# Performance work log

Hardware: AMD Instinct MI355X
Metric: run time of the kernel (lower is better)

Reference implementation:

```python
import jax, jax.numpy as jnp
import numpy as np

TOKENS, D_IN, D_OUT, RANK = 16384, 4096, 4096, 512

def setup_inputs() -> dict:
    key = jax.random.key(0)
    k1, k2, k3, k4 = jax.random.split(key, 4)
    x = jax.random.normal(k1, (TOKENS, D_IN), dtype=jnp.float32)
    U = jax.random.normal(k2, (D_OUT, RANK), dtype=jnp.float32) * 0.02
    sigma = jax.random.uniform(k3, (RANK,), dtype=jnp.float32)
    V = jax.random.normal(k4, (D_IN, RANK), dtype=jnp.float32) * 0.02
    return {"x": x, "U": U, "sigma": sigma, "V": V}

def reference(x, U, sigma, V):
    # W = U @ diag(sigma) @ V.T  (shape [out, in]); out = x @ W.T
    # diag(sigma) contraction expressed as a column scale of U (same math).
    W = (U * sigma[None, :]) @ V.T          # [out, in]
    return x @ W.T                          # [tokens, out]
```

## Files before the change

### kernel.cpp

```cpp
#include <hip/hip_runtime.h>

typedef __bf16 bf16;
typedef __bf16 bf16x4 __attribute__((ext_vector_type(4)));
typedef __bf16 bf16x8 __attribute__((ext_vector_type(8)));
typedef float  f32x4  __attribute__((ext_vector_type(4)));

#define TOKENS 16384
#define D_IN   4096
#define D_OUT  4096
#define RANK   512

__device__ inline void gload_lds16(const bf16* g, bf16* l) {
    __builtin_amdgcn_global_load_lds((const __attribute__((address_space(1))) void*)g,
                                     (__attribute__((address_space(3))) void*)l,
                                     16, 0, 0);
}

__global__ __launch_bounds__(256) void vt_scale(const float* __restrict__ V,
                                                const float* __restrict__ sg,
                                                bf16* __restrict__ Vst) {
    __shared__ float tile[64][65];
    const int tx = threadIdx.x & 63;
    const int ty = threadIdx.x >> 6;
    const int kb = blockIdx.x * 64;
    const int rb = blockIdx.y * 64;
    const float s = sg[rb + tx];
#pragma unroll
    for (int i = ty; i < 64; i += 4)
        tile[i][tx] = V[(size_t)(kb + i) * RANK + rb + tx] * s;
    __syncthreads();
#pragma unroll
    for (int i = ty; i < 64; i += 4) {
        int r = rb + i;
        int kp = kb + (tx ^ ((r & 7) << 3));
        Vst[(size_t)r * D_IN + kp] = (bf16)tile[tx][i];
    }
}

__global__ __launch_bounds__(256) void cvt_bf16_4(const float* __restrict__ in,
                                                  bf16* __restrict__ o, int n4) {
    int i = blockIdx.x * 256 + threadIdx.x;
    if (i < n4) {
        f32x4 v = *(const f32x4*)(in + (size_t)i * 4);
        bf16x4 b = { (bf16)v[0], (bf16)v[1], (bf16)v[2], (bf16)v[3] };
        *(bf16x4*)(o + (size_t)i * 4) = b;
    }
}

__global__ __launch_bounds__(256, 2) void gemm1_pipe(const float* __restrict__ A,
                                                     const bf16* __restrict__ B,
                                                     bf16* __restrict__ T,
                                                     int M, int N, int K) {
    __shared__ bf16 Al[2][128 * 64];
    __shared__ bf16 Bl[2][128 * 64];

    const int t  = threadIdx.x;
    const int l  = t & 63;
    const int w  = t >> 6;
    const int wr = w >> 1, wc = w & 1;
    const int lr = l & 15;
    const int kg = l >> 4;
    const int sxor = (l & 7) << 3;

    const int nwg = gridDim.x;
    const int bid = blockIdx.x;
    const int cpx = nwg >> 3;
    const int swz = (bid & 7) * cpx + (bid >> 3);
    const int ntn = N >> 7;
    const int tm  = (swz / ntn) << 7;
    const int tn  = (swz % ntn) << 7;

    const int arow  = t >> 4;
    const int acg   = t & 15;
    const int awxor = (arow & 7) << 3;
    const float* Ap = A + (size_t)(tm + arow) * K + acg * 4;
    const bf16* Bp  = B + (size_t)(tn + (t >> 3)) * K + (t & 7) * 8;

    f32x4 acc[4][4] = {};
    f32x4 ra[8];

#pragma unroll
    for (int c = 0; c < 8; ++c)
        ra[c] = *(const f32x4*)(Ap + (size_t)(c * 16) * K);
#pragma unroll
    for (int c = 0; c < 4; ++c)
        gload_lds16(Bp + (size_t)(c * 32) * K, &Bl[0][(c * 256 + t) * 8]);
#pragma unroll
    for (int c = 0; c < 8; ++c) {
        bf16x4 b = { (bf16)ra[c][0], (bf16)ra[c][1], (bf16)ra[c][2], (bf16)ra[c][3] };
        *(bf16x4*)&Al[0][(c * 16 + arow) * 64 + ((acg * 4) ^ awxor)] = b;
    }
    asm volatile("s_waitcnt vmcnt(0) lgkmcnt(0)" ::: "memory");
    __builtin_amdgcn_s_barrier();

    int cb = 0;
    for (int kt = 0; kt < K - 64; kt += 64) {
        const int nb = cb ^ 1;
#pragma unroll
        for (int c = 0; c < 8; ++c)
            ra[c] = *(const f32x4*)(Ap + kt + 64 + (size_t)(c * 16) * K);
#pragma unroll
        for (int c = 0; c < 4; ++c)
            gload_lds16(Bp + kt + 64 + (size_t)(c * 32) * K, &Bl[nb][(c * 256 + t) * 8]);

#pragma unroll
        for (int ks = 0; ks < 2; ++ks) {
            bf16x8 af[4], bfr[4];
#pragma unroll
            for (int f = 0; f < 4; ++f) {
                af[f]  = *(const bf16x8*)&Al[cb][(wr * 64 + f * 16 + lr) * 64 + ((ks * 32 + kg * 8) ^ sxor)];
                bfr[f] = *(const bf16x8*)&Bl[cb][(wc * 64 + f * 16 + lr) * 64 + ((ks * 32 + kg * 8) ^ sxor)];
            }
#pragma unroll
            for (int fm = 0; fm < 4; ++fm)
#pragma unroll
                for (int fn = 0; fn < 4; ++fn)
                    acc[fm][fn] = __builtin_amdgcn_mfma_f32_16x16x32_bf16(
                        af[fm], bfr[fn], acc[fm][fn], 0, 0, 0);
        }

#pragma unroll
        for (int c = 0; c < 8; ++c) {
            bf16x4 b = { (bf16)ra[c][0], (bf16)ra[c][1], (bf16)ra[c][2], (bf16)ra[c][3] };
            *(bf16x4*)&Al[nb][(c * 16 + arow) * 64 + ((acg * 4) ^ awxor)] = b;
        }
        asm volatile("s_waitcnt vmcnt(0) lgkmcnt(0)" ::: "memory");
        __builtin_amdgcn_s_barrier();
        cb = nb;
    }

#pragma unroll
    for (int ks = 0; ks < 2; ++ks) {
        bf16x8 af[4], bfr[4];
#pragma unroll
        for (int f = 0; f < 4; ++f) {
            af[f]  = *(const bf16x8*)&Al[cb][(wr * 64 + f * 16 + lr) * 64 + ((ks * 32 + kg * 8) ^ sxor)];
            bfr[f] = *(const bf16x8*)&Bl[cb][(wc * 64 + f * 16 + lr) * 64 + ((ks * 32 + kg * 8) ^ sxor)];
        }
#pragma unroll
        for (int fm = 0; fm < 4; ++fm)
#pragma unroll
            for (int fn = 0; fn < 4; ++fn)
                acc[fm][fn] = __builtin_amdgcn_mfma_f32_16x16x32_bf16(
                    af[fm], bfr[fn], acc[fm][fn], 0, 0, 0);
    }

    const int r0 = tm + wr * 64 + kg * 4;
    const int c0 = tn + wc * 64 + lr;
#pragma unroll
    for (int fm = 0; fm < 4; ++fm)
#pragma unroll
        for (int fn = 0; fn < 4; ++fn)
#pragma unroll
            for (int r = 0; r < 4; ++r)
                T[(size_t)(r0 + fm * 16 + r) * N + (c0 + fn * 16)] = (bf16)acc[fm][fn][r];
}

__global__ __launch_bounds__(256) void gemm2_bt(const bf16* __restrict__ A,
                                                const bf16* __restrict__ B,
                                                float* __restrict__ out,
                                                int M, int N, int K) {
    __shared__ bf16 Al[128 * 64];
    __shared__ bf16 Bl[128 * 64];

    const int t  = threadIdx.x;
    const int l  = t & 63;
    const int w  = t >> 6;
    const int wr = w >> 1, wc = w & 1;
    const int lr = l & 15;
    const int kg = l >> 4;

    const int nwg = gridDim.x;
    const int bid = blockIdx.x;
    const int cpx = nwg >> 3;
    const int swz = (bid & 7) * cpx + (bid >> 3);
    const int ntn = N >> 7;
    const int tm  = (swz / ntn) << 7;
    const int tn  = (swz % ntn) << 7;

    f32x4 acc[4][4] = {};

    for (int kt = 0; kt < K; kt += 64) {
#pragma unroll
        for (int c = 0; c < 4; ++c) {
            int i = c * 256 + t;
            gload_lds16(A + (size_t)(tm + (i >> 3)) * K + kt + (i & 7) * 8, &Al[i * 8]);
        }
#pragma unroll
        for (int c = 0; c < 4; ++c) {
            int i = c * 256 + t;
            gload_lds16(B + (size_t)(tn + (i >> 3)) * K + kt + (i & 7) * 8, &Bl[i * 8]);
        }
        __syncthreads();

#pragma unroll
        for (int ks = 0; ks < 2; ++ks) {
            bf16x8 af[4], bfr[4];
#pragma unroll
            for (int f = 0; f < 4; ++f) {
                af[f]  = *(const bf16x8*)&Al[(wr * 64 + f * 16 + lr) * 64 + ks * 32 + kg * 8];
                bfr[f] = *(const bf16x8*)&Bl[(wc * 64 + f * 16 + lr) * 64 + ks * 32 + kg * 8];
            }
#pragma unroll
            for (int fm = 0; fm < 4; ++fm)
#pragma unroll
                for (int fn = 0; fn < 4; ++fn)
                    acc[fm][fn] = __builtin_amdgcn_mfma_f32_16x16x32_bf16(
                        af[fm], bfr[fn], acc[fm][fn], 0, 0, 0);
        }
        __syncthreads();
    }

    const int r0 = tm + wr * 64 + kg * 4;
    const int c0 = tn + wc * 64 + lr;
#pragma unroll
    for (int fm = 0; fm < 4; ++fm)
#pragma unroll
        for (int fn = 0; fn < 4; ++fn)
#pragma unroll
            for (int r = 0; r < 4; ++r)
                out[(size_t)(r0 + fm * 16 + r) * N + (c0 + fn * 16)] = acc[fm][fn][r];
}

extern "C" void kernel_launch(void* const* d_in, const int* in_sizes, int n_in,
                              void* d_out, int out_size, void* d_ws, size_t ws_size,
                              hipStream_t stream) {
    const float* x  = (const float*)d_in[0];
    const float* U  = (const float*)d_in[1];
    const float* sg = (const float*)d_in[2];
    const float* V  = (const float*)d_in[3];
    float* out = (float*)d_out;

    char* ws = (char*)d_ws;
    bf16* Vst = (bf16*)ws;
    bf16* Ub  = (bf16*)(ws + (4u << 20));
    bf16* T   = (bf16*)(ws + (8u << 20));

    vt_scale<<<dim3(D_IN / 64, RANK / 64), 256, 0, stream>>>(V, sg, Vst);
    cvt_bf16_4<<<(D_OUT * RANK / 4 + 255) / 256, 256, 0, stream>>>(U, Ub, D_OUT * RANK / 4);

    gemm1_pipe<<<(TOKENS / 128) * (RANK / 128), 256, 0, stream>>>(
        x, Vst, T, TOKENS, RANK, D_IN);

    gemm2_bt<<<(TOKENS / 128) * (D_OUT / 128), 256, 0, stream>>>(
        T, Ub, out, TOKENS, D_OUT, RANK);
}
```

Baseline: 310.3 us.

## Deepen B prefetch to triple buffer in gemm1 and double-buffer gemm2

The first GEMM now keeps three LDS buffers for the bf16 B operand and prefetches two tiles ahead. It uses partial vmcnt waits so the newest B loads stay in flight across the barrier, and drops the occupancy hint from launch bounds. The second GEMM gains double-buffered LDS with the next tile's direct-to-LDS loads issued before the current tile's MFMAs, replacing the load, sync, compute, sync loop. This aims to hide global-load latency behind matrix math, at the cost of more LDS per block and possibly lower occupancy. The sxor change uses lr instead of l, which is the same value, so it does not change the swizzle.

```diff
diff --git a/kernel.cpp b/kernel.cpp
--- a/kernel.cpp
+++ b/kernel.cpp
@@ -47,12 +47,12 @@
     }
 }
 
-__global__ __launch_bounds__(256, 2) void gemm1_pipe(const float* __restrict__ A,
-                                                     const bf16* __restrict__ B,
-                                                     bf16* __restrict__ T,
-                                                     int M, int N, int K) {
+__global__ __launch_bounds__(256) void gemm1_cnt(const float* __restrict__ A,
+                                                 const bf16* __restrict__ B,
+                                                 bf16* __restrict__ T,
+                                                 int M, int N, int K) {
     __shared__ bf16 Al[2][128 * 64];
-    __shared__ bf16 Bl[2][128 * 64];
+    __shared__ bf16 Bl[3][128 * 64];
 
     const int t  = threadIdx.x;
     const int l  = t & 63;
@@ -60,7 +60,7 @@
     const int wr = w >> 1, wc = w & 1;
     const int lr = l & 15;
     const int kg = l >> 4;
-    const int sxor = (l & 7) << 3;
+    const int sxor = (lr & 7) << 3;
 
     const int nwg = gridDim.x;
     const int bid = blockIdx.x;
@@ -76,6 +76,8 @@
     const float* Ap = A + (size_t)(tm + arow) * K + acg * 4;
     const bf16* Bp  = B + (size_t)(tn + (t >> 3)) * K + (t & 7) * 8;
 
+    const int NT = K >> 6;
+
     f32x4 acc[4][4] = {};
     f32x4 ra[8];
 
@@ -85,31 +87,45 @@
 #pragma unroll
     for (int c = 0; c < 4; ++c)
         gload_lds16(Bp + (size_t)(c * 32) * K, &Bl[0][(c * 256 + t) * 8]);
+#pragma unroll
+    for (int c = 0; c < 4; ++c)
+        gload_lds16(Bp + 64 + (size_t)(c * 32) * K, &Bl[1][(c * 256 + t) * 8]);
 #pragma unroll
     for (int c = 0; c < 8; ++c) {
         bf16x4 b = { (bf16)ra[c][0], (bf16)ra[c][1], (bf16)ra[c][2], (bf16)ra[c][3] };
         *(bf16x4*)&Al[0][(c * 16 + arow) * 64 + ((acg * 4) ^ awxor)] = b;
     }
-    asm volatile("s_waitcnt vmcnt(0) lgkmcnt(0)" ::: "memory");
+    asm volatile("s_waitcnt vmcnt(4) lgkmcnt(0)" ::: "memory");
+    __builtin_amdgcn_sched_barrier(0);
     __builtin_amdgcn_s_barrier();
-
-    int cb = 0;
-    for (int kt = 0; kt < K - 64; kt += 64) {
-        const int nb = cb ^ 1;
-#pragma unroll
-        for (int c = 0; c < 8; ++c)
-            ra[c] = *(const f32x4*)(Ap + kt + 64 + (size_t)(c * 16) * K);
-#pragma unroll
-        for (int c = 0; c < 4; ++c)
-            gload_lds16(Bp + kt + 64 + (size_t)(c * 32) * K, &Bl[nb][(c * 256 + t) * 8]);
+    __builtin_amdgcn_sched_barrier(0);
+
+    int bb = 0;
+    for (int i = 0; i < NT; ++i) {
+        const int kt = i << 6;
+        const bf16* Alc = &Al[i & 1][0];
+        const bf16* Blc = &Bl[bb][0];
+        const int bb2 = (bb >= 1) ? bb - 1 : 2;
+
+        if (i + 1 < NT) {
+#pragma unroll
+            for (int c = 0; c < 8; ++c)
+                ra[c] = *(const f32x4*)(Ap + kt + 64 + (size_t)(c * 16) * K);
+        }
+        if (i + 2 < NT) {
+#pragma unroll
+            for (int c = 0; c < 4; ++c)
+                gload_lds16(Bp + kt + 128 + (size_t)(c * 32) * K,
+                            &Bl[bb2][(c * 256 + t) * 8]);
+        }
 
 #pragma unroll
         for (int ks = 0; ks < 2; ++ks) {
             bf16x8 af[4], bfr[4];
 #pragma unroll
             for (int f = 0; f < 4; ++f) {
-                af[f]  = *(const bf16x8*)&Al[cb][(wr * 64 + f * 16 + lr) * 64 + ((ks * 32 + kg * 8) ^ sxor)];
-                bfr[f] = *(const bf16x8*)&Bl[cb][(wc * 64 + f * 16 + lr) * 64 + ((ks * 32 + kg * 8) ^ sxor)];
+                af[f]  = *(const bf16x8*)&Alc[(wr * 64 + f * 16 + lr) * 64 + ((ks * 32 + kg * 8) ^ sxor)];
+                bfr[f] = *(const bf16x8*)&Blc[(wc * 64 + f * 16 + lr) * 64 + ((ks * 32 + kg * 8) ^ sxor)];
             }
 #pragma unroll
             for (int fm = 0; fm < 4; ++fm)
@@ -119,30 +135,21 @@
                         af[fm], bfr[fn], acc[fm][fn], 0, 0, 0);
         }
 
-#pragma unroll
-        for (int c = 0; c < 8; ++c) {
-            bf16x4 b = { (bf16)ra[c][0], (bf16)ra[c][1], (bf16)ra[c][2], (bf16)ra[c][3] };
-            *(bf16x4*)&Al[nb][(c * 16 + arow) * 64 + ((acg * 4) ^ awxor)] = b;
-        }
-        asm volatile("s_waitcnt vmcnt(0) lgkmcnt(0)" ::: "memory");
-        __builtin_amdgcn_s_barrier();
-        cb = nb;
-    }
-
-#pragma unroll
-    for (int ks = 0; ks < 2; ++ks) {
-        bf16x8 af[4], bfr[4];
-#pragma unroll
-        for (int f = 0; f < 4; ++f) {
-            af[f]  = *(const bf16x8*)&Al[cb][(wr * 64 + f * 16 + lr) * 64 + ((ks * 32 + kg * 8) ^ sxor)];
-            bfr[f] = *(const bf16x8*)&Bl[cb][(wc * 64 + f * 16 + lr) * 64 + ((ks * 32 + kg * 8) ^ sxor)];
-        }
-#pragma unroll
-        for (int fm = 0; fm < 4; ++fm)
-#pragma unroll
-            for (int fn = 0; fn < 4; ++fn)
-                acc[fm][fn] = __builtin_amdgcn_mfma_f32_16x16x32_bf16(
-                    af[fm], bfr[fn], acc[fm][fn], 0, 0, 0);
+        if (i + 1 < NT) {
+#pragma unroll
+            for (int c = 0; c < 8; ++c) {
+                bf16x4 b = { (bf16)ra[c][0], (bf16)ra[c][1], (bf16)ra[c][2], (bf16)ra[c][3] };
+                *(bf16x4*)&Al[(i + 1) & 1][(c * 16 + arow) * 64 + ((acg * 4) ^ awxor)] = b;
+            }
+            if (i + 2 < NT)
+                asm volatile("s_waitcnt vmcnt(4) lgkmcnt(0)" ::: "memory");
+            else
+                asm volatile("s_waitcnt vmcnt(0) lgkmcnt(0)" ::: "memory");
+            __builtin_amdgcn_sched_barrier(0);
+            __builtin_amdgcn_s_barrier();
+            __builtin_amdgcn_sched_barrier(0);
+        }
+        bb = (bb + 1 == 3) ? 0 : bb + 1;
     }
 
     const int r0 = tm + wr * 64 + kg * 4;
@@ -156,12 +163,12 @@
                 T[(size_t)(r0 + fm * 16 + r) * N + (c0 + fn * 16)] = (bf16)acc[fm][fn][r];
 }
 
-__global__ __launch_bounds__(256) void gemm2_bt(const bf16* __restrict__ A,
+__global__ __launch_bounds__(256) void gemm2_pf(const bf16* __restrict__ A,
                                                 const bf16* __restrict__ B,
                                                 float* __restrict__ out,
                                                 int M, int N, int K) {
-    __shared__ bf16 Al[128 * 64];
-    __shared__ bf16 Bl[128 * 64];
+    __shared__ bf16 Al[2][128 * 64];
+    __shared__ bf16 Bl[2][128 * 64];
 
     const int t  = threadIdx.x;
     const int l  = t & 63;
@@ -178,28 +185,39 @@
     const int tm  = (swz / ntn) << 7;
     const int tn  = (swz % ntn) << 7;
 
+    const bf16* Apt = A + (size_t)(tm + (t >> 3)) * K + (t & 7) * 8;
+    const bf16* Bpt = B + (size_t)(tn + (t >> 3)) * K + (t & 7) * 8;
+
+    const int NT = K >> 6;
+
     f32x4 acc[4][4] = {};
 
-    for (int kt = 0; kt < K; kt += 64) {
-#pragma unroll
-        for (int c = 0; c < 4; ++c) {
-            int i = c * 256 + t;
-            gload_lds16(A + (size_t)(tm + (i >> 3)) * K + kt + (i & 7) * 8, &Al[i * 8]);
-        }
-#pragma unroll
-        for (int c = 0; c < 4; ++c) {
-            int i = c * 256 + t;
-            gload_lds16(B + (size_t)(tn + (i >> 3)) * K + kt + (i & 7) * 8, &Bl[i * 8]);
-        }
-        __syncthreads();
-
+#pragma unroll
+    for (int c = 0; c < 4; ++c) {
+        gload_lds16(Apt + (size_t)(c * 32) * K, &Al[0][(c * 256 + t) * 8]);
+        gload_lds16(Bpt + (size_t)(c * 32) * K, &Bl[0][(c * 256 + t) * 8]);
+    }
+    asm volatile("s_waitcnt vmcnt(0)" ::: "memory");
+    __builtin_amdgcn_sched_barrier(0);
+    __builtin_amdgcn_s_barrier();
+    __builtin_amdgcn_sched_barrier(0);
+
+    for (int i = 0; i < NT; ++i) {
+        const int kt = i << 6;
+        if (i + 1 < NT) {
+#pragma unroll
+            for (int c = 0; c < 4; ++c) {
+                gload_lds16(Apt + kt + 64 + (size_t)(c * 32) * K, &Al[(i + 1) & 1][(c * 256 + t) * 8]);
+                gload_lds16(Bpt + kt + 64 + (size_t)(c * 32) * K, &Bl[(i + 1) & 1][(c * 256 + t) * 8]);
+            }
+        }
 #pragma unroll
         for (int ks = 0; ks < 2; ++ks) {
             bf16x8 af[4], bfr[4];
 #pragma unroll
             for (int f = 0; f < 4; ++f) {
-                af[f]  = *(const bf16x8*)&Al[(wr * 64 + f * 16 + lr) * 64 + ks * 32 + kg * 8];
-                bfr[f] = *(const bf16x8*)&Bl[(wc * 64 + f * 16 + lr) * 64 + ks * 32 + kg * 8];
+                af[f]  = *(const bf16x8*)&Al[i & 1][(wr * 64 + f * 16 + lr) * 64 + ks * 32 + kg * 8];
+                bfr[f] = *(const bf16x8*)&Bl[i & 1][(wc * 64 + f * 16 + lr) * 64 + ks * 32 + kg * 8];
             }
 #pragma unroll
             for (int fm = 0; fm < 4; ++fm)
@@ -208,7 +226,12 @@
                     acc[fm][fn] = __builtin_amdgcn_mfma_f32_16x16x32_bf16(
                         af[fm], bfr[fn], acc[fm][fn], 0, 0, 0);
         }
-        __syncthreads();
+        if (i + 1 < NT) {
+            asm volatile("s_waitcnt vmcnt(0)" ::: "memory");
+            __builtin_amdgcn_sched_barrier(0);
+            __builtin_amdgcn_s_barrier();
+            __builtin_amdgcn_sched_barrier(0);
+        }
     }
 
     const int r0 = tm + wr * 64 + kg * 4;
@@ -239,9 +262,9 @@
     vt_scale<<<dim3(D_IN / 64, RANK / 64), 256, 0, stream>>>(V, sg, Vst);
     cvt_bf16_4<<<(D_OUT * RANK / 4 + 255) / 256, 256, 0, stream>>>(U, Ub, D_OUT * RANK / 4);
 
-    gemm1_pipe<<<(TOKENS / 128) * (RANK / 128), 256, 0, stream>>>(
+    gemm1_cnt<<<(TOKENS / 128) * (RANK / 128), 256, 0, stream>>>(
         x, Vst, T, TOKENS, RANK, D_IN);
 
-    gemm2_bt<<<(TOKENS / 128) * (D_OUT / 128), 256, 0, stream>>>(
+    gemm2_pf<<<(TOKENS / 128) * (D_OUT / 128), 256, 0, stream>>>(
         T, Ub, out, TOKENS, D_OUT, RANK);
 }
```

Result: faster. 270.0 us (-13.0%).
